# Kernel optimization log

Hardware: AMD Instinct MI355X
Metric: run time of the kernel (lower is better)

## Reference

```python
import jax, jax.numpy as jnp
import numpy as np

H, K_CHUNKS = 16, 16          # z_num = (h, k)
Z_DIM = 64
OC, IC, KW = 128, 128, 3      # per-chunk out, in, kernel width
HID = 256
O, I = H * OC, K_CHUNKS * IC  # 2048, 2048
L = 3
N_PDE, D_PDE = 1024, 64


def setup_inputs() -> dict:
    key = jax.random.key(0)
    ks = jax.random.split(key, 10)
    def rn(k, shape, scale=1.0):
        return jax.random.normal(k, shape, dtype=jnp.float32) * scale
    return {
        "Z": rn(ks[0], (H * K_CHUNKS, Z_DIM)),                 # stacked z_list (fmod(randn,2) ~ randn)
        "z_bias": rn(ks[1], (O,)),
        "unet_1d_weights": rn(ks[2], (O, I, L), 0.02),
        "unet_1d_bias": rn(ks[3], (O,), 0.02),
        "pde_inputs": rn(ks[4], (N_PDE, D_PDE)),
        "W1": rn(ks[5], (Z_DIM, HID), 1.0 / np.sqrt(Z_DIM)),
        "U1": rn(ks[6], (D_PDE, HID), 1.0 / np.sqrt(D_PDE)),
        "b1": jnp.zeros((HID,), jnp.float32),
        "W2": rn(ks[7], (HID, OC * IC * KW), 1.0 / np.sqrt(HID)),
        "b2": jnp.zeros((OC * IC * KW,), jnp.float32),
    }


def reference(Z, z_bias, unet_1d_weights, unet_1d_bias, pde_inputs, W1, U1, b1, W2, b2):
    # Batched hypernet: replaces the h*k sequential hyper_net calls.
    pde_feat = pde_inputs.mean(axis=0) @ U1                    # [HID], shared conditioning
    hidden = jnp.tanh(Z @ W1 + pde_feat + b1)                  # [h*k, HID]
    w = (hidden @ W2 + b2).reshape(H, K_CHUNKS, OC, IC, KW)    # per-chunk weights
    # cat over j along dim=1 (in-channels), then over i along dim=0 (out-channels)
    exe_unet_weight = w.transpose(0, 2, 1, 3, 4).reshape(O, I, KW)  # [O, I, K]
    w_2d = jnp.einsum('oik,oil->oikl', exe_unet_weight, unet_1d_weights)  # [O, I, K, L]
    bb = z_bias + unet_1d_bias                                 # [O]
    return (w_2d, bb)
```

## Files before the change

### kernel.cpp

```cpp
#include <hip/hip_runtime.h>
#include <hip/hip_bf16.h>
#include <math.h>

#define ZD_ 64
#define HID_ 256
#define NW2_ 49152
#define W2D_OUT 37748736

typedef short bf16x8 __attribute__((ext_vector_type(8)));
typedef float f32x4 __attribute__((ext_vector_type(4)));

static __device__ __forceinline__ unsigned short f2bf(float f) {
    union { float f; unsigned u; } v; v.f = f;
    unsigned r = v.u + 0x7FFF + ((v.u >> 16) & 1);
    return (unsigned short)(r >> 16);
}

static __device__ __forceinline__ unsigned pack2(float lo, float hi) {
    return (unsigned)f2bf(lo) | ((unsigned)f2bf(hi) << 16);
}

__global__ void prep_kernel(const float* __restrict__ Z,
                            const float* __restrict__ pde,
                            const float* __restrict__ W1,
                            const float* __restrict__ U1,
                            const float* __restrict__ b1,
                            const float* __restrict__ z_bias,
                            const float* __restrict__ u_bias,
                            unsigned short* __restrict__ hiddenA,
                            float* __restrict__ out_bb) {
    __shared__ float part[16][64];
    __shared__ float meanv[64];
    __shared__ float zr[64];
    const int t = threadIdx.x, m = blockIdx.x;
    if (t < 64) zr[t] = Z[m * ZD_ + t];
    const int c4 = t & 15, rg = t >> 4;
    float sx = 0.f, sy = 0.f, sz = 0.f, sw = 0.f;
    const float4* p = (const float4*)pde;
    for (int r = 0; r < 64; ++r) {
        float4 v = p[(rg * 64 + r) * 16 + c4];
        sx += v.x; sy += v.y; sz += v.z; sw += v.w;
    }
    part[rg][c4 * 4 + 0] = sx; part[rg][c4 * 4 + 1] = sy;
    part[rg][c4 * 4 + 2] = sz; part[rg][c4 * 4 + 3] = sw;
    __syncthreads();
    if (t < 64) {
        float a = 0.f;
        #pragma unroll
        for (int g = 0; g < 16; ++g) a += part[g][t];
        meanv[t] = a * (1.f / 1024.f);
    }
    __syncthreads();
    float f = b1[t];
    #pragma unroll
    for (int d = 0; d < 64; ++d) f = fmaf(meanv[d], U1[d * HID_ + t], f);
    float s = f;
    #pragma unroll
    for (int d = 0; d < 64; ++d) s = fmaf(zr[d], W1[d * HID_ + t], s);
    hiddenA[((size_t)(t >> 3) * 256 + m) * 8 + (t & 7)] = f2bf(tanhf(s));
    if (m < 8) {
        const int idx = m * 256 + t;
        out_bb[idx] = z_bias[idx] + u_bias[idx];
    }
}

#define BT_S2 132
#define WL_ST 97
#define WL_SZ 1552

__global__ __launch_bounds__(512, 4)
void gemm_expand(const unsigned short* __restrict__ hiddenA,
                 const float* __restrict__ W2,
                 const float* __restrict__ b2,
                 const float* __restrict__ unet,
                 float* __restrict__ out) {
    __shared__ unsigned bT[96 * BT_S2];

    const int t = threadIdx.x;
    const int lane = t & 63;
    const int wave = t >> 6;
    const int n15 = lane & 15;
    const int quad = lane >> 4;
    const int L = lane & 31;
    const int half = lane >> 5;
    const int oc = blockIdx.x >> 2;
    const int icq = blockIdx.x & 3;
    const int n0g = oc * 384 + icq * 96;

    #pragma unroll
    for (int i = 0; i < 6; ++i) {
        const int u  = i * 512 + t;
        const int kp = u / 24;
        const int nq = u - kp * 24;
        const float* p0 = W2 + (size_t)(2 * kp) * NW2_ + n0g + nq * 4;
        const float4 va = *(const float4*)p0;
        const float4 vb = *(const float4*)(p0 + NW2_);
        const int kpx = kp ^ ((nq & 7) << 1) ^ (((nq >> 3) & 1) << 4);
        unsigned* r0 = &bT[(4 * nq) * BT_S2 + kpx];
        r0[0 * BT_S2] = pack2(va.x, vb.x);
        r0[1 * BT_S2] = pack2(va.y, vb.y);
        r0[2 * BT_S2] = pack2(va.z, vb.z);
        r0[3 * BT_S2] = pack2(va.w, vb.w);
    }
    __syncthreads();

    f32x4 acc[2][6];
    #pragma unroll
    for (int a = 0; a < 2; ++a)
        #pragma unroll
        for (int b = 0; b < 6; ++b) acc[a][b] = (f32x4){0.f, 0.f, 0.f, 0.f};

    #pragma unroll
    for (int ks = 0; ks < 8; ++ks) {
        const int g = ks * 4 + quad;
        bf16x8 afr[2];
        #pragma unroll
        for (int mi = 0; mi < 2; ++mi)
            afr[mi] = *(const bf16x8*)(hiddenA +
                      ((size_t)g * 256 + (wave * 2 + mi) * 16 + n15) * 8);
        const int base4 = ks * 16 + quad * 4;
        #pragma unroll
        for (int nt = 0; nt < 6; ++nt) {
            const int n = nt * 16 + n15;
            const int nqr = n >> 2;
            const int swz = ((nqr & 7) << 1) ^ (((nqr >> 3) & 1) << 4);
            const unsigned* row = &bT[n * BT_S2];
            union { bf16x8 v; unsigned long long q[2]; } bb;
            bb.q[0] = *(const unsigned long long*)&row[(base4)     ^ swz];
            bb.q[1] = *(const unsigned long long*)&row[(base4 + 2) ^ swz];
            acc[0][nt] = __builtin_amdgcn_mfma_f32_16x16x32_bf16(afr[0], bb.v, acc[0][nt], 0, 0, 0);
            acc[1][nt] = __builtin_amdgcn_mfma_f32_16x16x32_bf16(afr[1], bb.v, acc[1][nt], 0, 0, 0);
        }
    }

    float gb2v[6];
    #pragma unroll
    for (int nt = 0; nt < 6; ++nt) gb2v[nt] = b2[n0g + nt * 16 + n15];

    __syncthreads();

    float* wl = ((float*)bT) + wave * WL_SZ;

    #pragma unroll
    for (int mi = 0; mi < 2; ++mi) {
        #pragma unroll
        for (int nt = 0; nt < 6; ++nt)
            #pragma unroll
            for (int r = 0; r < 4; ++r)
                wl[(quad * 4 + r) * WL_ST + nt * 16 + n15] = acc[mi][nt][r] + gb2v[nt];

        const int o = (wave * 2 + mi) * 128 + oc;
        const float* uo = unet + (size_t)o * 6144;
        float* ob = out + (size_t)o * 18432;

        #pragma unroll
        for (int kp = 0; kp < 8; ++kp) {
            const int kc = kp * 2 + half;
            const float* wrow = wl + kc * WL_ST;
            const float* ub = uo + kc * 384 + icq * 96;
            float* os = ob + kc * 1152 + icq * 288;
            #pragma unroll
            for (int j = 0; j < 9; ++j) {
                const int d  = j * 32 + L;
                const int d3 = d / 3;
                const int d9 = d / 9;
                const int l  = d - 3 * d3;
                __builtin_nontemporal_store(wrow[d3] * ub[d9 * 3 + l], os + d);
            }
        }
    }
}

extern "C" void kernel_launch(void* const* d_in, const int* in_sizes, int n_in,
                              void* d_out, int out_size, void* d_ws, size_t ws_size,
                              hipStream_t stream) {
    const float* Z       = (const float*)d_in[0];
    const float* z_bias  = (const float*)d_in[1];
    const float* unet_w  = (const float*)d_in[2];
    const float* unet_b  = (const float*)d_in[3];
    const float* pde     = (const float*)d_in[4];
    const float* W1      = (const float*)d_in[5];
    const float* U1      = (const float*)d_in[6];
    const float* b1      = (const float*)d_in[7];
    const float* W2      = (const float*)d_in[8];
    const float* b2      = (const float*)d_in[9];
    float* out = (float*)d_out;

    unsigned short* hiddenA = (unsigned short*)d_ws;

    prep_kernel<<<256, 256, 0, stream>>>(Z, pde, W1, U1, b1, z_bias, unet_b,
                                         hiddenA, out + W2D_OUT);
    gemm_expand<<<512, 512, 0, stream>>>(hiddenA, W2, b2, unet_w, out);
}
```

Baseline: 284.5 us.

## Split gemm_expand M across two blocks, halve LDS with K chunking, raise occupancy

Doubles the grid so each block handles half the M rows (one 16-row tile per wave) and stages W2 in two K-chunks through a half-size LDS buffer. The epilogue staging is split into two passes to fit the smaller buffer, and launch bounds now ask for 8 blocks per CU to hide memory latency. W2 is now loaded and converted twice as often overall because each N-tile is read by two blocks. Nontemporal stores are also swapped for plain stores, which changes cache behaviour on the large output write.

```diff
diff --git a/kernel.cpp b/kernel.cpp
--- a/kernel.cpp
+++ b/kernel.cpp
@@ -64,17 +64,17 @@
     }
 }
 
-#define BT_S2 132
+#define BT_SC 68
 #define WL_ST 97
-#define WL_SZ 1552
+#define WL_SZ 776
 
-__global__ __launch_bounds__(512, 4)
+__global__ __launch_bounds__(512, 8)
 void gemm_expand(const unsigned short* __restrict__ hiddenA,
                  const float* __restrict__ W2,
                  const float* __restrict__ b2,
                  const float* __restrict__ unet,
                  float* __restrict__ out) {
-    __shared__ unsigned bT[96 * BT_S2];
+    __shared__ unsigned bT[96 * BT_SC];
 
     const int t = threadIdx.x;
     const int lane = t & 63;
@@ -83,80 +83,81 @@
     const int quad = lane >> 4;
     const int L = lane & 31;
     const int half = lane >> 5;
-    const int oc = blockIdx.x >> 2;
-    const int icq = blockIdx.x & 3;
+    const int mh  = blockIdx.x & 1;
+    const int icq = (blockIdx.x >> 1) & 3;
+    const int oc  = blockIdx.x >> 3;
     const int n0g = oc * 384 + icq * 96;
+    const int mt  = mh * 8 + wave;
 
+    f32x4 acc[6];
     #pragma unroll
-    for (int i = 0; i < 6; ++i) {
-        const int u  = i * 512 + t;
-        const int kp = u / 24;
-        const int nq = u - kp * 24;
-        const float* p0 = W2 + (size_t)(2 * kp) * NW2_ + n0g + nq * 4;
-        const float4 va = *(const float4*)p0;
-        const float4 vb = *(const float4*)(p0 + NW2_);
-        const int kpx = kp ^ ((nq & 7) << 1) ^ (((nq >> 3) & 1) << 4);
-        unsigned* r0 = &bT[(4 * nq) * BT_S2 + kpx];
-        r0[0 * BT_S2] = pack2(va.x, vb.x);
-        r0[1 * BT_S2] = pack2(va.y, vb.y);
-        r0[2 * BT_S2] = pack2(va.z, vb.z);
-        r0[3 * BT_S2] = pack2(va.w, vb.w);
-    }
-    __syncthreads();
+    for (int b = 0; b < 6; ++b) acc[b] = (f32x4){0.f, 0.f, 0.f, 0.f};
 
-    f32x4 acc[2][6];
-    #pragma unroll
-    for (int a = 0; a < 2; ++a)
+    for (int c = 0; c < 2; ++c) {
         #pragma unroll
-        for (int b = 0; b < 6; ++b) acc[a][b] = (f32x4){0.f, 0.f, 0.f, 0.f};
+        for (int i = 0; i < 3; ++i) {
+            const int u   = i * 512 + t;
+            const int kpl = u / 24;
+            const int nq  = u - kpl * 24;
+            const int kg  = c * 128 + 2 * kpl;
+            const float* p0 = W2 + (size_t)kg * NW2_ + n0g + nq * 4;
+            const float4 va = *(const float4*)p0;
+            const float4 vb = *(const float4*)(p0 + NW2_);
+            const int kpx = kpl ^ ((nq & 7) << 1) ^ (((nq >> 3) & 1) << 4);
+            unsigned* r0 = &bT[(4 * nq) * BT_SC + kpx];
+            r0[0 * BT_SC] = pack2(va.x, vb.x);
+            r0[1 * BT_SC] = pack2(va.y, vb.y);
+            r0[2 * BT_SC] = pack2(va.z, vb.z);
+            r0[3 * BT_SC] = pack2(va.w, vb.w);
+        }
+        __syncthreads();
 
-    #pragma unroll
-    for (int ks = 0; ks < 8; ++ks) {
-        const int g = ks * 4 + quad;
-        bf16x8 afr[2];
         #pragma unroll
-        for (int mi = 0; mi < 2; ++mi)
-            afr[mi] = *(const bf16x8*)(hiddenA +
-                      ((size_t)g * 256 + (wave * 2 + mi) * 16 + n15) * 8);
-        const int base4 = ks * 16 + quad * 4;
-        #pragma unroll
-        for (int nt = 0; nt < 6; ++nt) {
-            const int n = nt * 16 + n15;
-            const int nqr = n >> 2;
-            const int swz = ((nqr & 7) << 1) ^ (((nqr >> 3) & 1) << 4);
-            const unsigned* row = &bT[n * BT_S2];
-            union { bf16x8 v; unsigned long long q[2]; } bb;
-            bb.q[0] = *(const unsigned long long*)&row[(base4)     ^ swz];
-            bb.q[1] = *(const unsigned long long*)&row[(base4 + 2) ^ swz];
-            acc[0][nt] = __builtin_amdgcn_mfma_f32_16x16x32_bf16(afr[0], bb.v, acc[0][nt], 0, 0, 0);
-            acc[1][nt] = __builtin_amdgcn_mfma_f32_16x16x32_bf16(afr[1], bb.v, acc[1][nt], 0, 0, 0);
+        for (int ksl = 0; ksl < 4; ++ksl) {
+            const int g = (c * 4 + ksl) * 4 + quad;
+            const bf16x8 afr = *(const bf16x8*)(hiddenA +
+                      ((size_t)g * 256 + mt * 16 + n15) * 8);
+            const int base4 = ksl * 16 + quad * 4;
+            #pragma unroll
+            for (int nt = 0; nt < 6; ++nt) {
+                const int n = nt * 16 + n15;
+                const int nqr = n >> 2;
+                const int swz = ((nqr & 7) << 1) ^ (((nqr >> 3) & 1) << 4);
+                const unsigned* row = &bT[n * BT_SC];
+                union { bf16x8 v; unsigned long long q[2]; } bb;
+                bb.q[0] = *(const unsigned long long*)&row[(base4)     ^ swz];
+                bb.q[1] = *(const unsigned long long*)&row[(base4 + 2) ^ swz];
+                acc[nt] = __builtin_amdgcn_mfma_f32_16x16x32_bf16(afr, bb.v, acc[nt], 0, 0, 0);
+            }
         }
+        __syncthreads();
     }
 
     float gb2v[6];
     #pragma unroll
     for (int nt = 0; nt < 6; ++nt) gb2v[nt] = b2[n0g + nt * 16 + n15];
 
-    __syncthreads();
-
     float* wl = ((float*)bT) + wave * WL_SZ;
 
+    const int o = mt * 128 + oc;
+    const float* uo = unet + (size_t)o * 6144;
+    float* ob = out + (size_t)o * 18432;
+
     #pragma unroll
-    for (int mi = 0; mi < 2; ++mi) {
-        #pragma unroll
-        for (int nt = 0; nt < 6; ++nt)
+    for (int p = 0; p < 2; ++p) {
+        if ((quad >> 1) == p) {
             #pragma unroll
-            for (int r = 0; r < 4; ++r)
-                wl[(quad * 4 + r) * WL_ST + nt * 16 + n15] = acc[mi][nt][r] + gb2v[nt];
-
-        const int o = (wave * 2 + mi) * 128 + oc;
-        const float* uo = unet + (size_t)o * 6144;
-        float* ob = out + (size_t)o * 18432;
+            for (int nt = 0; nt < 6; ++nt)
+                #pragma unroll
+                for (int r = 0; r < 4; ++r)
+                    wl[((quad & 1) * 4 + r) * WL_ST + nt * 16 + n15] = acc[nt][r] + gb2v[nt];
+        }
 
         #pragma unroll
-        for (int kp = 0; kp < 8; ++kp) {
-            const int kc = kp * 2 + half;
-            const float* wrow = wl + kc * WL_ST;
+        for (int kp = 0; kp < 4; ++kp) {
+            const int r8 = kp * 2 + half;
+            const int kc = p * 8 + r8;
+            const float* wrow = wl + r8 * WL_ST;
             const float* ub = uo + kc * 384 + icq * 96;
             float* os = ob + kc * 1152 + icq * 288;
             #pragma unroll
@@ -165,7 +166,7 @@
                 const int d3 = d / 3;
                 const int d9 = d / 9;
                 const int l  = d - 3 * d3;
-                __builtin_nontemporal_store(wrow[d3] * ub[d9 * 3 + l], os + d);
+                os[d] = wrow[d3] * ub[d9 * 3 + l];
             }
         }
     }
@@ -190,5 +191,5 @@
 
     prep_kernel<<<256, 256, 0, stream>>>(Z, pde, W1, U1, b1, z_bias, unet_b,
                                          hiddenA, out + W2D_OUT);
-    gemm_expand<<<512, 512, 0, stream>>>(hiddenA, W2, b2, unet_w, out);
+    gemm_expand<<<1024, 512, 0, stream>>>(hiddenA, W2, b2, unet_w, out);
 }
```

Result: slower. 354.2 us (+24.5%).

## Double threads per block, one M tile per wave, two-pass epilogue staging

Applied to the files above, without the earlier changes.

The expand kernel now launches 1024 threads per block, so each wave owns a single 16-row M tile instead of two. This halves the accumulator registers per wave and aims to put more waves in flight on the store-bound epilogue. The LDS staging buffer per wave is halved, so the epilogue runs in two passes of 8 k-rows each. The nontemporal output stores become ordinary stores, which changes how the large output stream interacts with the caches. The aggressive launch bound may push register pressure or cause spills.

```diff
diff --git a/kernel.cpp b/kernel.cpp
--- a/kernel.cpp
+++ b/kernel.cpp
@@ -66,9 +66,9 @@
 
 #define BT_S2 132
 #define WL_ST 97
-#define WL_SZ 1552
+#define WL_SZ 776
 
-__global__ __launch_bounds__(512, 4)
+__global__ __launch_bounds__(1024, 8)
 void gemm_expand(const unsigned short* __restrict__ hiddenA,
                  const float* __restrict__ W2,
                  const float* __restrict__ b2,
@@ -86,10 +86,11 @@
     const int oc = blockIdx.x >> 2;
     const int icq = blockIdx.x & 3;
     const int n0g = oc * 384 + icq * 96;
+    const int mt = wave;
 
     #pragma unroll
-    for (int i = 0; i < 6; ++i) {
-        const int u  = i * 512 + t;
+    for (int i = 0; i < 3; ++i) {
+        const int u  = i * 1024 + t;
         const int kp = u / 24;
         const int nq = u - kp * 24;
         const float* p0 = W2 + (size_t)(2 * kp) * NW2_ + n0g + nq * 4;
@@ -104,20 +105,15 @@
     }
     __syncthreads();
 
-    f32x4 acc[2][6];
+    f32x4 acc[6];
     #pragma unroll
-    for (int a = 0; a < 2; ++a)
-        #pragma unroll
-        for (int b = 0; b < 6; ++b) acc[a][b] = (f32x4){0.f, 0.f, 0.f, 0.f};
+    for (int b = 0; b < 6; ++b) acc[b] = (f32x4){0.f, 0.f, 0.f, 0.f};
 
     #pragma unroll
     for (int ks = 0; ks < 8; ++ks) {
         const int g = ks * 4 + quad;
-        bf16x8 afr[2];
-        #pragma unroll
-        for (int mi = 0; mi < 2; ++mi)
-            afr[mi] = *(const bf16x8*)(hiddenA +
-                      ((size_t)g * 256 + (wave * 2 + mi) * 16 + n15) * 8);
+        const bf16x8 afr = *(const bf16x8*)(hiddenA +
+                  ((size_t)g * 256 + mt * 16 + n15) * 8);
         const int base4 = ks * 16 + quad * 4;
         #pragma unroll
         for (int nt = 0; nt < 6; ++nt) {
@@ -128,8 +124,7 @@
             union { bf16x8 v; unsigned long long q[2]; } bb;
             bb.q[0] = *(const unsigned long long*)&row[(base4)     ^ swz];
             bb.q[1] = *(const unsigned long long*)&row[(base4 + 2) ^ swz];
-            acc[0][nt] = __builtin_amdgcn_mfma_f32_16x16x32_bf16(afr[0], bb.v, acc[0][nt], 0, 0, 0);
-            acc[1][nt] = __builtin_amdgcn_mfma_f32_16x16x32_bf16(afr[1], bb.v, acc[1][nt], 0, 0, 0);
+            acc[nt] = __builtin_amdgcn_mfma_f32_16x16x32_bf16(afr, bb.v, acc[nt], 0, 0, 0);
         }
     }
 
@@ -141,22 +136,25 @@
 
     float* wl = ((float*)bT) + wave * WL_SZ;
 
+    const int o = mt * 128 + oc;
+    const float* uo = unet + (size_t)o * 6144;
+    float* ob = out + (size_t)o * 18432;
+
     #pragma unroll
-    for (int mi = 0; mi < 2; ++mi) {
-        #pragma unroll
-        for (int nt = 0; nt < 6; ++nt)
+    for (int p = 0; p < 2; ++p) {
+        if ((quad >> 1) == p) {
             #pragma unroll
-            for (int r = 0; r < 4; ++r)
-                wl[(quad * 4 + r) * WL_ST + nt * 16 + n15] = acc[mi][nt][r] + gb2v[nt];
-
-        const int o = (wave * 2 + mi) * 128 + oc;
-        const float* uo = unet + (size_t)o * 6144;
-        float* ob = out + (size_t)o * 18432;
+            for (int nt = 0; nt < 6; ++nt)
+                #pragma unroll
+                for (int r = 0; r < 4; ++r)
+                    wl[((quad & 1) * 4 + r) * WL_ST + nt * 16 + n15] = acc[nt][r] + gb2v[nt];
+        }
 
         #pragma unroll
-        for (int kp = 0; kp < 8; ++kp) {
-            const int kc = kp * 2 + half;
-            const float* wrow = wl + kc * WL_ST;
+        for (int kp = 0; kp < 4; ++kp) {
+            const int r8 = kp * 2 + half;
+            const int kc = p * 8 + r8;
+            const float* wrow = wl + r8 * WL_ST;
             const float* ub = uo + kc * 384 + icq * 96;
             float* os = ob + kc * 1152 + icq * 288;
             #pragma unroll
@@ -165,7 +163,7 @@
                 const int d3 = d / 3;
                 const int d9 = d / 9;
                 const int l  = d - 3 * d3;
-                __builtin_nontemporal_store(wrow[d3] * ub[d9 * 3 + l], os + d);
+                os[d] = wrow[d3] * ub[d9 * 3 + l];
             }
         }
     }
@@ -190,5 +188,5 @@
 
     prep_kernel<<<256, 256, 0, stream>>>(Z, pde, W1, U1, b1, z_bias, unet_b,
                                          hiddenA, out + W2D_OUT);
-    gemm_expand<<<512, 512, 0, stream>>>(hiddenA, W2, b2, unet_w, out);
+    gemm_expand<<<512, 1024, 0, stream>>>(hiddenA, W2, b2, unet_w, out);
 }
```

Measured after the change: 325.9 us. 1.15x slower.
